# Kernel optimization log

Measured on AMD Instinct MI355X. Metric: run time of the kernel, lower is better.

Reference implementation:

```python
import jax, jax.numpy as jnp
import numpy as np

N_QUBITS = 8  # circuit width; must be <= embed_dim


def setup_inputs() -> dict:
    key = jax.random.key(0)
    k_x, k_th, k_w1, k_w2 = jax.random.split(key, 4)
    B, T, C, F = 4, 4096, 1024, 4096
    return {
        "x": jax.random.normal(k_x, (B, T, C), dtype=jnp.float32),
        "circuit_params": jax.random.normal(k_th, (N_QUBITS,), dtype=jnp.float32),
        "w1": jax.random.normal(k_w1, (F, N_QUBITS), dtype=jnp.float32) / np.sqrt(N_QUBITS).astype(np.float32),
        "b1": jnp.zeros((F,), dtype=jnp.float32),
        "w2": jax.random.normal(k_w2, (C, F), dtype=jnp.float32) / np.sqrt(F).astype(np.float32),
        "b2": jnp.zeros((C,), dtype=jnp.float32),
    }


def reference(x, circuit_params, w1, b1, w2, b2):
    # Closed-form simulation of the per-token circuit:
    #   RX(x_w) on each wire -> <Z_w> = cos(x_w)  (product state)
    #   RZ(theta_w) leaves <Z> (and products of Z's) invariant
    #   CNOT ladder (w -> w+1) maps Z_w -> Z_0 Z_1 ... Z_w (Heisenberg)
    # => <Z_w>_final = prod_{k<=w} cos(x_k)  : a cumulative product.
    q = jnp.cumprod(jnp.cos(x[..., :N_QUBITS]), axis=-1)  # [B, T, n_qubits]
    h = jax.nn.relu(jnp.einsum("btq,fq->btf", q, w1) + b1)  # [B, T, ffn_dim]
    out = jnp.einsum("btf,cf->btc", h, w2) + b2              # [B, T, embed_dim]
    # keep a dependence on circuit_params with zero value, matching its (null)
    # contribution while keeping it in the graph
    return out + (circuit_params.sum() * 0.0)
```

## Files before the change

### kernel.cpp

```cpp
#include <hip/hip_runtime.h>
#include <hip/hip_bf16.h>
#include <cmath>


typedef __attribute__((ext_vector_type(8))) __bf16 bf16x8;
typedef __attribute__((ext_vector_type(4))) float f32x4;
typedef __attribute__((ext_vector_type(8))) unsigned short ushortx8;

#define GAS __attribute__((address_space(1)))
#define LAS __attribute__((address_space(3)))

__device__ __forceinline__ unsigned short f32_to_bf16(float f) {
    union { float f; unsigned int u; } v; v.f = f;
    unsigned int u = v.u;
    u += 0x7FFFu + ((u >> 16) & 1u);
    return (unsigned short)(u >> 16);
}

__global__ __launch_bounds__(256) void cvt_w2(const float* __restrict__ src,
                                              unsigned short* __restrict__ dst) {
    int i = blockIdx.x * 256 + threadIdx.x;
    const float4* s = reinterpret_cast<const float4*>(src);
    float4 a = s[2 * i], b = s[2 * i + 1];
    ushortx8 o;
    o[0] = f32_to_bf16(a.x); o[1] = f32_to_bf16(a.y);
    o[2] = f32_to_bf16(a.z); o[3] = f32_to_bf16(a.w);
    o[4] = f32_to_bf16(b.x); o[5] = f32_to_bf16(b.y);
    o[6] = f32_to_bf16(b.z); o[7] = f32_to_bf16(b.w);
    reinterpret_cast<ushortx8*>(dst)[i] = o;
}

__global__ __launch_bounds__(256) void h_kernel(const float* __restrict__ x,
                                                const float* __restrict__ w1,
                                                const float* __restrict__ b1,
                                                unsigned short* __restrict__ H) {
    constexpr int C = 1024, F = 4096, TOK = 32;
    __shared__ float qs[TOK][8];
    const int tid = threadIdx.x;
    const int tb  = blockIdx.x & 511;
    const int fb  = blockIdx.x >> 9;
    const int t0  = tb * TOK;
    const int f0  = fb * 2048 + tid * 8;

    if (tid < TOK) {
        const float* xr = x + (size_t)(t0 + tid) * C;
        float p = 1.0f;
        #pragma unroll
        for (int j = 0; j < 8; ++j) { p *= cosf(xr[j]); qs[tid][j] = p; }
    }

    float w[8][8]; float bb[8];
    #pragma unroll
    for (int u = 0; u < 8; ++u) {
        const float4* wp = reinterpret_cast<const float4*>(w1 + (size_t)(f0 + u) * 8);
        float4 a = wp[0], c = wp[1];
        w[u][0] = a.x; w[u][1] = a.y; w[u][2] = a.z; w[u][3] = a.w;
        w[u][4] = c.x; w[u][5] = c.y; w[u][6] = c.z; w[u][7] = c.w;
        bb[u] = b1[f0 + u];
    }
    __syncthreads();

    for (int tt = 0; tt < TOK; ++tt) {
        float q[8];
        #pragma unroll
        for (int j = 0; j < 8; ++j) q[j] = qs[tt][j];
        ushortx8 o;
        #pragma unroll
        for (int u = 0; u < 8; ++u) {
            float acc = bb[u];
            #pragma unroll
            for (int j = 0; j < 8; ++j) acc += q[j] * w[u][j];
            o[u] = f32_to_bf16(fmaxf(acc, 0.0f));
        }
        *reinterpret_cast<ushortx8*>(H + (size_t)(t0 + tt) * F + f0) = o;
    }
}

__global__ __launch_bounds__(512, 2) void gemm256(const unsigned short* __restrict__ A,
                                                  const unsigned short* __restrict__ B,
                                                  const float* __restrict__ bias,
                                                  float* __restrict__ C) {
    constexpr int M = 16384, N = 1024, K = 4096;
    constexpr int BM = 256, BN = 256, BK = 64;
    constexpr int NKT = K / BK;

    __shared__ __align__(16) unsigned short lds[2][2][2][128 * 64];

    const int tid  = threadIdx.x;
    const int wv   = tid >> 6;
    const int lane = tid & 63;
    const int wr   = wv >> 2;
    const int wc   = wv & 3;
    const int rl   = lane & 15;
    const int kq4  = lane >> 4;

    const int bid = blockIdx.x;
    const int wg  = (bid & 7) * 32 + (bid >> 3);
    const int tm  = wg & 63;
    const int tn  = wg >> 6;
    const int rowBase = tm * BM;
    const int colBase = tn * BN;

    const int i0 = tid >> 3;
    const int sw = ((tid & 7) ^ (i0 & 7)) * 8;
    const unsigned short* pA0 = A + (size_t)(rowBase + i0) * K + sw;
    const unsigned short* pA1 = A + (size_t)(rowBase + i0 + 128) * K + sw;
    const int bR0 = (i0 & 31) + ((i0 >> 5) << 6);
    const unsigned short* pB0 = B + (size_t)(colBase + bR0) * K + sw;
    const unsigned short* pB1 = B + (size_t)(colBase + bR0 + 128) * K + sw;

#define STAGE_A(HH, BB, KT)  do {                                                   \
    __builtin_amdgcn_global_load_lds((const GAS unsigned int*)(const void*)          \
        (pA0 + (size_t)(HH) * 64 * K + (KT) * 64),                                   \
        (LAS unsigned int*)(void*)&lds[BB][0][HH][tid * 8], 16, 0, 0);               \
    __builtin_amdgcn_global_load_lds((const GAS unsigned int*)(const void*)          \
        (pA1 + (size_t)(HH) * 64 * K + (KT) * 64),                                   \
        (LAS unsigned int*)(void*)&lds[BB][0][HH][4096 + tid * 8], 16, 0, 0);        \
} while (0)
#define STAGE_B(HH, BB, KT)  do {                                                   \
    __builtin_amdgcn_global_load_lds((const GAS unsigned int*)(const void*)          \
        (pB0 + (size_t)(HH) * 32 * K + (KT) * 64),                                   \
        (LAS unsigned int*)(void*)&lds[BB][1][HH][tid * 8], 16, 0, 0);               \
    __builtin_amdgcn_global_load_lds((const GAS unsigned int*)(const void*)          \
        (pB1 + (size_t)(HH) * 32 * K + (KT) * 64),                                   \
        (LAS unsigned int*)(void*)&lds[BB][1][HH][4096 + tid * 8], 16, 0, 0);        \
} while (0)

    const int ch0  = ((0 + kq4) ^ (rl & 7)) * 8;
    const int ch1  = ((4 + kq4) ^ (rl & 7)) * 8;
    const int aOff = (wr * 64 + rl) * 64;
    const int bOff = (wc * 32 + rl) * 64;

    bf16x8 aF[4][2], bF0[2][2], bF1[2][2];
    f32x4 acc[8][4];
    #pragma unroll
    for (int m = 0; m < 8; ++m)
        #pragma unroll
        for (int n = 0; n < 4; ++n) acc[m][n] = (f32x4){0.f, 0.f, 0.f, 0.f};

#define LOAD_A(HH) { _Pragma("unroll")                                               \
    for (int m_ = 0; m_ < 4; ++m_) {                                                 \
        aF[m_][0] = *(const bf16x8*)&lds[b][0][HH][aOff + m_ * 1024 + ch0];          \
        aF[m_][1] = *(const bf16x8*)&lds[b][0][HH][aOff + m_ * 1024 + ch1]; } }
#define LOAD_B(DST, HH) { _Pragma("unroll")                                          \
    for (int n_ = 0; n_ < 2; ++n_) {                                                 \
        DST[n_][0] = *(const bf16x8*)&lds[b][1][HH][bOff + n_ * 1024 + ch0];         \
        DST[n_][1] = *(const bf16x8*)&lds[b][1][HH][bOff + n_ * 1024 + ch1]; } }
#define MFMA_QUAD(BF, MO, NO) { _Pragma("unroll")                                    \
    for (int m_ = 0; m_ < 4; ++m_) { _Pragma("unroll")                               \
        for (int n_ = 0; n_ < 2; ++n_) {                                             \
            acc[MO + m_][NO + n_] = __builtin_amdgcn_mfma_f32_16x16x32_bf16(         \
                aF[m_][0], BF[n_][0], acc[MO + m_][NO + n_], 0, 0, 0);               \
            acc[MO + m_][NO + n_] = __builtin_amdgcn_mfma_f32_16x16x32_bf16(         \
                aF[m_][1], BF[n_][1], acc[MO + m_][NO + n_], 0, 0, 0); } } }
#define PHASE_TAIL(MFMAS) do {                                                       \
    __builtin_amdgcn_s_barrier();                                                    \
    asm volatile("s_waitcnt lgkmcnt(0)" ::: "memory");                               \
    __builtin_amdgcn_sched_barrier(0);                                               \
    __builtin_amdgcn_s_setprio(1);                                                   \
    MFMAS                                                                            \
    __builtin_amdgcn_s_setprio(0);                                                   \
    __builtin_amdgcn_sched_barrier(0);                                               \
    asm volatile("s_waitcnt vmcnt(6)" ::: "memory");                                 \
    __builtin_amdgcn_s_barrier();                                                    \
    __builtin_amdgcn_sched_barrier(0);                                               \
} while (0)

    STAGE_A(0, 0, 0);
    STAGE_B(1, 0, 0);
    STAGE_B(0, 0, 0);
    STAGE_A(1, 0, 0);
    STAGE_A(0, 1, 1);
    STAGE_B(1, 1, 1);
    asm volatile("s_waitcnt vmcnt(6)" ::: "memory");
    __builtin_amdgcn_s_barrier();
    __builtin_amdgcn_sched_barrier(0);

    #pragma unroll 2
    for (int kt = 0; kt < NKT; ++kt) {
        const int b = kt & 1;
        LOAD_A(0); LOAD_B(bF0, 0);
        if (kt < NKT - 1) STAGE_B(0, b ^ 1, kt + 1);
        PHASE_TAIL(MFMA_QUAD(bF0, 0, 0));
        LOAD_B(bF1, 1);
        if (kt < NKT - 1) STAGE_A(1, b ^ 1, kt + 1);
        PHASE_TAIL(MFMA_QUAD(bF1, 0, 2));
        LOAD_A(1);
        if (kt < NKT - 2) STAGE_A(0, b, kt + 2);
        PHASE_TAIL(MFMA_QUAD(bF1, 4, 2));
        if (kt < NKT - 2) STAGE_B(1, b, kt + 2);
        PHASE_TAIL(MFMA_QUAD(bF0, 4, 0));
    }

    const int rq = lane >> 4;
    #pragma unroll
    for (int n = 0; n < 4; ++n) {
        const int col = colBase + wc * 64 + n * 16 + rl;
        const float bv = bias[col];
        #pragma unroll
        for (int m = 0; m < 8; ++m) {
            #pragma unroll
            for (int j = 0; j < 4; ++j) {
                const int row = rowBase + wr * 128 + m * 16 + rq * 4 + j;
                C[(size_t)row * N + col] = acc[m][n][j] + bv;
            }
        }
    }
#undef STAGE_A
#undef STAGE_B
#undef LOAD_A
#undef LOAD_B
#undef MFMA_QUAD
#undef PHASE_TAIL
}

extern "C" void kernel_launch(void* const* d_in, const int* in_sizes, int n_in,
                              void* d_out, int out_size, void* d_ws, size_t ws_size,
                              hipStream_t stream) {
    const float* x  = (const float*)d_in[0];
    const float* w1 = (const float*)d_in[2];
    const float* b1 = (const float*)d_in[3];
    const float* w2 = (const float*)d_in[4];
    const float* b2 = (const float*)d_in[5];
    float* out = (float*)d_out;

    constexpr int M = 16384;
    constexpr int N = 1024;
    constexpr int K = 4096;

    unsigned short* Hbuf = (unsigned short*)d_ws;
    unsigned short* w2bf = (unsigned short*)((char*)d_ws + (size_t)M * K * 2);

    cvt_w2<<<(N * K) / (256 * 8), 256, 0, stream>>>(w2, w2bf);
    h_kernel<<<(M / 32) * 2, 256, 0, stream>>>(x, w1, b1, Hbuf);
    gemm256<<<(M / 256) * (N / 256), 512, 0, stream>>>(Hbuf, w2bf, b2, out);
}
```

Measured before the change: 261.8 us.

## Fuse H computation into GEMM prologue, generating A tiles on the fly in LDS

Drops the separate h_kernel and the 128 MB bf16 H buffer. Each GEMM block computes the cumprod-cos features for its 256 rows, streams w1/b1 slices into LDS, and builds the relu(q·w1+b1) A tiles directly in shared memory inside the pipelined K loop. This removes the global write and re-read of H and one kernel launch. In exchange the work is recomputed once per N-tile (4x redundancy), there is extra VALU work interleaved with the MFMA phases, more LDS is used, and the block-to-tile mapping is changed to group rows per XCD.

```diff
diff --git a/kernel.cpp b/kernel.cpp
--- a/kernel.cpp
+++ b/kernel.cpp
@@ -30,61 +30,19 @@
     reinterpret_cast<ushortx8*>(dst)[i] = o;
 }
 
-__global__ __launch_bounds__(256) void h_kernel(const float* __restrict__ x,
-                                                const float* __restrict__ w1,
-                                                const float* __restrict__ b1,
-                                                unsigned short* __restrict__ H) {
-    constexpr int C = 1024, F = 4096, TOK = 32;
-    __shared__ float qs[TOK][8];
-    const int tid = threadIdx.x;
-    const int tb  = blockIdx.x & 511;
-    const int fb  = blockIdx.x >> 9;
-    const int t0  = tb * TOK;
-    const int f0  = fb * 2048 + tid * 8;
-
-    if (tid < TOK) {
-        const float* xr = x + (size_t)(t0 + tid) * C;
-        float p = 1.0f;
-        #pragma unroll
-        for (int j = 0; j < 8; ++j) { p *= cosf(xr[j]); qs[tid][j] = p; }
-    }
-
-    float w[8][8]; float bb[8];
-    #pragma unroll
-    for (int u = 0; u < 8; ++u) {
-        const float4* wp = reinterpret_cast<const float4*>(w1 + (size_t)(f0 + u) * 8);
-        float4 a = wp[0], c = wp[1];
-        w[u][0] = a.x; w[u][1] = a.y; w[u][2] = a.z; w[u][3] = a.w;
-        w[u][4] = c.x; w[u][5] = c.y; w[u][6] = c.z; w[u][7] = c.w;
-        bb[u] = b1[f0 + u];
-    }
-    __syncthreads();
-
-    for (int tt = 0; tt < TOK; ++tt) {
-        float q[8];
-        #pragma unroll
-        for (int j = 0; j < 8; ++j) q[j] = qs[tt][j];
-        ushortx8 o;
-        #pragma unroll
-        for (int u = 0; u < 8; ++u) {
-            float acc = bb[u];
-            #pragma unroll
-            for (int j = 0; j < 8; ++j) acc += q[j] * w[u][j];
-            o[u] = f32_to_bf16(fmaxf(acc, 0.0f));
-        }
-        *reinterpret_cast<ushortx8*>(H + (size_t)(t0 + tt) * F + f0) = o;
-    }
-}
-
-__global__ __launch_bounds__(512, 2) void gemm256(const unsigned short* __restrict__ A,
-                                                  const unsigned short* __restrict__ B,
-                                                  const float* __restrict__ bias,
-                                                  float* __restrict__ C) {
+__global__ __launch_bounds__(512, 2) void gemm_fused(const float* __restrict__ x,
+                                                     const float* __restrict__ w1,
+                                                     const float* __restrict__ b1,
+                                                     const unsigned short* __restrict__ B,
+                                                     const float* __restrict__ bias,
+                                                     float* __restrict__ C) {
     constexpr int M = 16384, N = 1024, K = 4096;
     constexpr int BM = 256, BN = 256, BK = 64;
     constexpr int NKT = K / BK;
 
     __shared__ __align__(16) unsigned short lds[2][2][2][128 * 64];
+    __shared__ float qs[256][8];
+    __shared__ float w1s[2][576];
 
     const int tid  = threadIdx.x;
     const int wv   = tid >> 6;
@@ -95,28 +53,19 @@
     const int kq4  = lane >> 4;
 
     const int bid = blockIdx.x;
-    const int wg  = (bid & 7) * 32 + (bid >> 3);
-    const int tm  = wg & 63;
-    const int tn  = wg >> 6;
+    const int xcd = bid & 7;
+    const int loc = bid >> 3;
+    const int tm  = xcd * 8 + (loc & 7);
+    const int tn  = loc >> 3;
     const int rowBase = tm * BM;
     const int colBase = tn * BN;
 
-    const int i0 = tid >> 3;
-    const int sw = ((tid & 7) ^ (i0 & 7)) * 8;
-    const unsigned short* pA0 = A + (size_t)(rowBase + i0) * K + sw;
-    const unsigned short* pA1 = A + (size_t)(rowBase + i0 + 128) * K + sw;
+    const int i0  = tid >> 3;
+    const int sw8 = ((tid & 7) ^ (i0 & 7)) * 8;
     const int bR0 = (i0 & 31) + ((i0 >> 5) << 6);
-    const unsigned short* pB0 = B + (size_t)(colBase + bR0) * K + sw;
-    const unsigned short* pB1 = B + (size_t)(colBase + bR0 + 128) * K + sw;
-
-#define STAGE_A(HH, BB, KT)  do {                                                   \
-    __builtin_amdgcn_global_load_lds((const GAS unsigned int*)(const void*)          \
-        (pA0 + (size_t)(HH) * 64 * K + (KT) * 64),                                   \
-        (LAS unsigned int*)(void*)&lds[BB][0][HH][tid * 8], 16, 0, 0);               \
-    __builtin_amdgcn_global_load_lds((const GAS unsigned int*)(const void*)          \
-        (pA1 + (size_t)(HH) * 64 * K + (KT) * 64),                                   \
-        (LAS unsigned int*)(void*)&lds[BB][0][HH][4096 + tid * 8], 16, 0, 0);        \
-} while (0)
+    const unsigned short* pB0 = B + (size_t)(colBase + bR0) * K + sw8;
+    const unsigned short* pB1 = B + (size_t)(colBase + bR0 + 128) * K + sw8;
+
 #define STAGE_B(HH, BB, KT)  do {                                                   \
     __builtin_amdgcn_global_load_lds((const GAS unsigned int*)(const void*)          \
         (pB0 + (size_t)(HH) * 32 * K + (KT) * 64),                                   \
@@ -124,6 +73,41 @@
     __builtin_amdgcn_global_load_lds((const GAS unsigned int*)(const void*)          \
         (pB1 + (size_t)(HH) * 32 * K + (KT) * 64),                                   \
         (LAS unsigned int*)(void*)&lds[BB][1][HH][4096 + tid * 8], 16, 0, 0);        \
+} while (0)
+
+#define STAGE_W(SLOT, KT)  do {                                                     \
+    __builtin_amdgcn_global_load_lds((const GAS unsigned int*)(const void*)          \
+        (w1 + (size_t)((KT) * 64 + (tid & 63)) * 8 + (tid >> 6)),                    \
+        (LAS unsigned int*)(void*)&w1s[SLOT][tid], 4, 0, 0);                         \
+    __builtin_amdgcn_global_load_lds((const GAS unsigned int*)(const void*)          \
+        (b1 + (KT) * 64 + lane),                                                     \
+        (LAS unsigned int*)(void*)&w1s[SLOT][512 + lane], 4, 0, 0);                  \
+} while (0)
+
+#define COMPUTE_A(HH, BB, SLOT) do {                                                 \
+    const int r0_ = (HH) * 64 + i0;                                                  \
+    f32x4 q0a = *(const f32x4*)&qs[r0_][0],       q0b = *(const f32x4*)&qs[r0_][4];  \
+    f32x4 q1a = *(const f32x4*)&qs[r0_ + 128][0], q1b = *(const f32x4*)&qs[r0_ + 128][4]; \
+    f32x4 bba = *(const f32x4*)&w1s[SLOT][512 + sw8];                                \
+    f32x4 bbb = *(const f32x4*)&w1s[SLOT][512 + sw8 + 4];                            \
+    float a0_[8], a1_[8];                                                            \
+    _Pragma("unroll") for (int u = 0; u < 4; ++u) {                                  \
+        a0_[u] = bba[u]; a0_[4 + u] = bbb[u];                                        \
+        a1_[u] = bba[u]; a1_[4 + u] = bbb[u]; }                                      \
+    _Pragma("unroll") for (int j = 0; j < 8; ++j) {                                  \
+        f32x4 wA = *(const f32x4*)&w1s[SLOT][j * 64 + sw8];                          \
+        f32x4 wB = *(const f32x4*)&w1s[SLOT][j * 64 + sw8 + 4];                      \
+        float qj0 = (j < 4) ? q0a[j & 3] : q0b[j & 3];                               \
+        float qj1 = (j < 4) ? q1a[j & 3] : q1b[j & 3];                               \
+        _Pragma("unroll") for (int u = 0; u < 4; ++u) {                              \
+            a0_[u] += qj0 * wA[u]; a0_[4 + u] += qj0 * wB[u];                        \
+            a1_[u] += qj1 * wA[u]; a1_[4 + u] += qj1 * wB[u]; } }                    \
+    bf16x8 h0_, h1_;                                                                 \
+    _Pragma("unroll") for (int u = 0; u < 8; ++u) {                                  \
+        h0_[u] = (__bf16)fmaxf(a0_[u], 0.0f);                                        \
+        h1_[u] = (__bf16)fmaxf(a1_[u], 0.0f); }                                      \
+    *reinterpret_cast<bf16x8*>(&lds[BB][0][HH][tid * 8]) = h0_;                      \
+    *reinterpret_cast<bf16x8*>(&lds[BB][0][HH][4096 + tid * 8]) = h1_;               \
 } while (0)
 
     const int ch0  = ((0 + kq4) ^ (rl & 7)) * 8;
@@ -153,7 +137,9 @@
                 aF[m_][0], BF[n_][0], acc[MO + m_][NO + n_], 0, 0, 0);               \
             acc[MO + m_][NO + n_] = __builtin_amdgcn_mfma_f32_16x16x32_bf16(         \
                 aF[m_][1], BF[n_][1], acc[MO + m_][NO + n_], 0, 0, 0); } } }
-#define PHASE_TAIL(MFMAS) do {                                                       \
+#define VM4 asm volatile("s_waitcnt vmcnt(4)" ::: "memory");
+#define VM6 asm volatile("s_waitcnt vmcnt(6)" ::: "memory");
+#define PHASE_TAIL(MFMAS, VMW) do {                                                  \
     __builtin_amdgcn_s_barrier();                                                    \
     asm volatile("s_waitcnt lgkmcnt(0)" ::: "memory");                               \
     __builtin_amdgcn_sched_barrier(0);                                               \
@@ -161,35 +147,50 @@
     MFMAS                                                                            \
     __builtin_amdgcn_s_setprio(0);                                                   \
     __builtin_amdgcn_sched_barrier(0);                                               \
-    asm volatile("s_waitcnt vmcnt(6)" ::: "memory");                                 \
+    asm volatile("s_waitcnt lgkmcnt(0)" ::: "memory");                               \
+    VMW                                                                              \
     __builtin_amdgcn_s_barrier();                                                    \
     __builtin_amdgcn_sched_barrier(0);                                               \
 } while (0)
 
-    STAGE_A(0, 0, 0);
+    if (tid < 256) {
+        const float* xr = x + (size_t)(rowBase + tid) * 1024;
+        float p = 1.0f;
+        #pragma unroll
+        for (int j = 0; j < 8; ++j) { p *= cosf(xr[j]); qs[tid][j] = p; }
+    }
+    __syncthreads();
+
+    STAGE_W(0, 0);
+    STAGE_B(0, 0, 0);
     STAGE_B(1, 0, 0);
-    STAGE_B(0, 0, 0);
-    STAGE_A(1, 0, 0);
-    STAGE_A(0, 1, 1);
-    STAGE_B(1, 1, 1);
+    STAGE_W(1, 1);
     asm volatile("s_waitcnt vmcnt(6)" ::: "memory");
     __builtin_amdgcn_s_barrier();
     __builtin_amdgcn_sched_barrier(0);
+    COMPUTE_A(0, 0, 0);
+    COMPUTE_A(1, 0, 0);
+    asm volatile("s_waitcnt lgkmcnt(0)" ::: "memory");
+    asm volatile("s_waitcnt vmcnt(4)" ::: "memory");
+    __builtin_amdgcn_s_barrier();
+    __builtin_amdgcn_sched_barrier(0);
 
     #pragma unroll 2
     for (int kt = 0; kt < NKT; ++kt) {
-        const int b = kt & 1;
+        const int b   = kt & 1;
+        const int nb  = b ^ 1;
+        const int kt1 = (kt + 1) & 63;
+        const int kt2 = (kt + 2) & 63;
         LOAD_A(0); LOAD_B(bF0, 0);
-        if (kt < NKT - 1) STAGE_B(0, b ^ 1, kt + 1);
-        PHASE_TAIL(MFMA_QUAD(bF0, 0, 0));
+        STAGE_B(0, nb, kt1);
+        PHASE_TAIL(MFMA_QUAD(bF0, 0, 0);, VM4);
         LOAD_B(bF1, 1);
-        if (kt < NKT - 1) STAGE_A(1, b ^ 1, kt + 1);
-        PHASE_TAIL(MFMA_QUAD(bF1, 0, 2));
+        STAGE_B(1, nb, kt1);
+        STAGE_W(b, kt2);
+        PHASE_TAIL(MFMA_QUAD(bF1, 0, 2);, VM6);
         LOAD_A(1);
-        if (kt < NKT - 2) STAGE_A(0, b, kt + 2);
-        PHASE_TAIL(MFMA_QUAD(bF1, 4, 2));
-        if (kt < NKT - 2) STAGE_B(1, b, kt + 2);
-        PHASE_TAIL(MFMA_QUAD(bF0, 4, 0));
+        PHASE_TAIL(MFMA_QUAD(bF1, 4, 2); COMPUTE_A(0, nb, nb);, );
+        PHASE_TAIL(MFMA_QUAD(bF0, 4, 0); COMPUTE_A(1, nb, nb);, VM4);
     }
 
     const int rq = lane >> 4;
@@ -206,12 +207,15 @@
             }
         }
     }
-#undef STAGE_A
 #undef STAGE_B
+#undef STAGE_W
+#undef COMPUTE_A
 #undef LOAD_A
 #undef LOAD_B
 #undef MFMA_QUAD
 #undef PHASE_TAIL
+#undef VM4
+#undef VM6
 }
 
 extern "C" void kernel_launch(void* const* d_in, const int* in_sizes, int n_in,
@@ -228,10 +232,8 @@
     constexpr int N = 1024;
     constexpr int K = 4096;
 
-    unsigned short* Hbuf = (unsigned short*)d_ws;
-    unsigned short* w2bf = (unsigned short*)((char*)d_ws + (size_t)M * K * 2);
+    unsigned short* w2bf = (unsigned short*)d_ws;
 
     cvt_w2<<<(N * K) / (256 * 8), 256, 0, stream>>>(w2, w2bf);
-    h_kernel<<<(M / 32) * 2, 256, 0, stream>>>(x, w1, b1, Hbuf);
-    gemm256<<<(M / 256) * (N / 256), 512, 0, stream>>>(Hbuf, w2bf, b2, out);
-}
+    gemm_fused<<<(M / 256) * (N / 256), 512, 0, stream>>>(x, w1, b1, w2bf, b2, out);
+}
```

Result: slower. 398.6 us (+52.3%).
